# Kernel optimization log

Measured on AMD Instinct MI355X. Metric: run time of the kernel, lower is better.

## Reference

```python
import jax, jax.numpy as jnp
import numpy as np

N_NODES = 100000
N_EDGES = 3200000
D_FEAT = 128
HIDDEN = 128
BN_EPS = 1e-3  # Keras BatchNormalization default epsilon


def setup_inputs() -> dict:
    key = jax.random.key(0)
    k = jax.random.split(key, 8)
    H = jax.random.normal(k[0], (N_NODES, D_FEAT), dtype=jnp.float32)
    edge_src = jax.random.randint(k[1], (N_EDGES,), 0, N_NODES, dtype=jnp.int32)
    edge_dst = jax.random.randint(k[2], (N_EDGES,), 0, N_NODES, dtype=jnp.int32)
    edge_w = jax.random.uniform(k[3], (N_EDGES,), dtype=jnp.float32)
    # BatchNorm (inference-mode) parameters
    gamma = jnp.ones((D_FEAT,), dtype=jnp.float32)
    beta = jnp.zeros((D_FEAT,), dtype=jnp.float32)
    moving_mean = 0.1 * jax.random.normal(k[4], (D_FEAT,), dtype=jnp.float32)
    moving_var = jnp.abs(1.0 + 0.1 * jax.random.normal(k[5], (D_FEAT,), dtype=jnp.float32))
    # Dense layer params
    W = jax.random.normal(k[6], (D_FEAT, HIDDEN), dtype=jnp.float32) / np.sqrt(D_FEAT)
    b = jnp.zeros((HIDDEN,), dtype=jnp.float32)
    return {
        "H": H, "edge_src": edge_src, "edge_dst": edge_dst, "edge_w": edge_w,
        "gamma": gamma, "beta": beta, "moving_mean": moving_mean,
        "moving_var": moving_var, "W": W, "b": b, "num_nodes": N_NODES,
    }


def reference(H, edge_src, edge_dst, edge_w, gamma, beta, moving_mean, moving_var, W, b, num_nodes):
    # Sparse adjacency SpMM: h[dst] += w * H[src]
    msgs = H[edge_src] * edge_w[:, None]                      # [E, d]
    h = jax.ops.segment_sum(msgs, edge_dst, num_segments=num_nodes)  # [N, d]
    # BatchNorm (inference) -> Dropout (identity at inference) -> Dense + exact GELU
    h = (h - moving_mean) * jax.lax.rsqrt(moving_var + BN_EPS) * gamma + beta
    out = jax.nn.gelu(h @ W + b, approximate=False)           # [N, hidden]
    return out
```

## Files before the change

### kernel.cpp

```cpp
#include <hip/hip_runtime.h>
#include <math.h>


#define DF 128
#define SCAN_ELEMS 2048
#define BKSH 6
#define BKNODES (1 << BKSH)
#define NB 256
#define CAP 4096
#define CAP2 3072
#define PBLOCKS 512

typedef short short8 __attribute__((ext_vector_type(8)));
typedef float f32x4 __attribute__((ext_vector_type(4)));

__device__ __forceinline__ unsigned short f32_to_bf16_rne(float f) {
  unsigned u = __float_as_uint(f);
  return (unsigned short)((u + 0x7FFFu + ((u >> 16) & 1u)) >> 16);
}

__global__ __launch_bounds__(256) void scatter_kernel(
    const float* __restrict__ H, const int* __restrict__ esrc,
    const int* __restrict__ edst, const float* __restrict__ ew,
    float* __restrict__ h, int E) {
  int tid = blockIdx.x * blockDim.x + threadIdx.x;
  int e = tid >> 5;
  int lane = tid & 31;
  if (e >= E) return;
  int s = esrc[e];
  int d = edst[e];
  float w = ew[e];
  const float4* Hs = reinterpret_cast<const float4*>(H + (size_t)s * DF);
  float4 v = Hs[lane];
  float* hd = h + (size_t)d * DF + lane * 4;
  atomicAdd(hd + 0, v.x * w);
  atomicAdd(hd + 1, v.y * w);
  atomicAdd(hd + 2, v.z * w);
  atomicAdd(hd + 3, v.w * w);
}

__global__ __launch_bounds__(256) void prep_all_kernel(
    const float4* __restrict__ H4, ushort4* __restrict__ Hb, int n4,
    const float* __restrict__ W, const float* __restrict__ gamma,
    const float* __restrict__ beta, const float* __restrict__ mean,
    const float* __restrict__ var, const float* __restrict__ b,
    unsigned short* __restrict__ W2frag, float* __restrict__ bias2) {
  int idx = blockIdx.x * blockDim.x + threadIdx.x;
  if (idx < n4) {
    float4 v = H4[idx];
    ushort4 o;
    o.x = f32_to_bf16_rne(v.x);
    o.y = f32_to_bf16_rne(v.y);
    o.z = f32_to_bf16_rne(v.z);
    o.w = f32_to_bf16_rne(v.w);
    Hb[idx] = o;
  }
  if (idx < 16384) {
    int i = idx & 7;
    int l = (idx >> 3) & 63;
    int kt = (idx >> 9) & 3;
    int ct = idx >> 11;
    int k = kt * 32 + (l >> 4) * 8 + i;
    int c = ct * 16 + (l & 15);
    float s = gamma[k] * rsqrtf(var[k] + 1e-3f);
    W2frag[idx] = f32_to_bf16_rne(s * W[(size_t)k * DF + c]);
  } else if (idx < 16384 + DF) {
    int c = idx - 16384;
    float acc = b[c];
    for (int k = 0; k < DF; ++k) {
      float s = gamma[k] * rsqrtf(var[k] + 1e-3f);
      float t = beta[k] - mean[k] * s;
      acc += t * W[(size_t)k * DF + c];
    }
    bias2[c] = acc;
  }
}

__global__ __launch_bounds__(512) void hist_blk_kernel(
    const int* __restrict__ edst, int* __restrict__ gbase,
    int E, int nbk, int chunk) {
  extern __shared__ int hcnt[];
  int bblk = blockIdx.x;
  int t = threadIdx.x;
  for (int i = t; i < nbk; i += 512) hcnt[i] = 0;
  __syncthreads();
  int e0 = bblk * chunk;
  int e1 = min(E, e0 + chunk);
  for (int e = e0 + t; e < e1; e += 512)
    atomicAdd(&hcnt[edst[e] >> BKSH], 1);
  __syncthreads();
  for (int k = t; k < nbk; k += 512)
    gbase[(size_t)k * NB + bblk] = hcnt[k];
}

__global__ __launch_bounds__(256) void scan1_kernel(
    int* __restrict__ data, int* __restrict__ bsum, int n) {
  __shared__ int s[256];
  int t = threadIdx.x;
  int base = blockIdx.x * SCAN_ELEMS + t * 8;
  int v[8];
  int tsum = 0;
#pragma unroll
  for (int k = 0; k < 8; ++k) {
    v[k] = (base + k < n) ? data[base + k] : 0;
    tsum += v[k];
  }
  s[t] = tsum;
  __syncthreads();
  for (int off = 1; off < 256; off <<= 1) {
    int tmp = (t >= off) ? s[t - off] : 0;
    __syncthreads();
    s[t] += tmp;
    __syncthreads();
  }
  int run = s[t] - tsum;
#pragma unroll
  for (int k = 0; k < 8; ++k) {
    if (base + k < n) data[base + k] = run;
    run += v[k];
  }
  if (t == 255) bsum[blockIdx.x] = s[255];
}

__global__ __launch_bounds__(256) void scan23_kernel(
    int* __restrict__ data, const int* __restrict__ bsum, int n, int nbA) {
  __shared__ int s[256];
  int t = threadIdx.x;
  int v = (t < nbA) ? bsum[t] : 0;
  s[t] = v;
  __syncthreads();
  for (int off = 1; off < 256; off <<= 1) {
    int tmp = (t >= off) ? s[t - off] : 0;
    __syncthreads();
    s[t] += tmp;
    __syncthreads();
  }
  int i = blockIdx.x * 256 + t;
  if (i < n) {
    int blk = i >> 11;
    int add = (blk == 0) ? 0 : s[blk - 1];
    data[i] += add;
  }
  if (blockIdx.x == 0 && t == 0) data[n] = s[nbA - 1];
}

__global__ __launch_bounds__(512) void scatter_blk_kernel(
    const int* __restrict__ esrc, const int* __restrict__ edst,
    const float* __restrict__ ew, const int* __restrict__ gbase,
    uint2* __restrict__ payload, int E, int nbk, int chunk) {
  extern __shared__ int cur[];
  int bblk = blockIdx.x;
  int t = threadIdx.x;
  for (int k = t; k < nbk; k += 512) cur[k] = gbase[(size_t)k * NB + bblk];
  __syncthreads();
  int e0 = bblk * chunk;
  int e1 = min(E, e0 + chunk);
  for (int e = e0 + t; e < e1; e += 512) {
    int d = edst[e];
    int k = d >> BKSH;
    int pos = atomicAdd(&cur[k], 1);
    uint2 v;
    v.x = (unsigned)esrc[e] | ((unsigned)(d & (BKNODES - 1)) << 17);
    v.y = __float_as_uint(ew[e]);
    payload[pos] = v;
  }
}

__global__ __launch_bounds__(1024, 8) void reorder_pull_kernel(
    const unsigned* __restrict__ Hb, const uint2* __restrict__ payload,
    const int* __restrict__ gbase, unsigned* __restrict__ hb_out,
    int* __restrict__ ctr, int N, int nbk) {
  __shared__ uint2 sorted[CAP2];
  __shared__ int cnt[BKNODES];
  __shared__ int scn[BKNODES];
  __shared__ int cur[BKNODES];
  __shared__ int s_bk;
  int t = threadIdx.x;
  int wid = t >> 6;
  int lane = t & 63;
  int half = lane >> 5;
  int sub = lane & 31;
  const uint2* __restrict__ Hb2 = (const uint2*)Hb;

  for (;;) {
    if (t == 0) s_bk = atomicAdd(ctr, 1);
    __syncthreads();
    int bk = s_bk;
    if (bk >= nbk) return;
    int base = gbase[(size_t)bk * NB];
    int end  = gbase[(size_t)(bk + 1) * NB];
    int len = end - base;

    if (len <= CAP2) {
      if (t < BKNODES) cnt[t] = 0;
      __syncthreads();
      for (int j = t; j < len; j += 1024)
        atomicAdd(&cnt[payload[base + j].x >> 17], 1);
      __syncthreads();
      if (t < BKNODES) scn[t] = cnt[t];
      __syncthreads();
      for (int off = 1; off < BKNODES; off <<= 1) {
        int tmp = (t < BKNODES && t >= off) ? scn[t - off] : 0;
        __syncthreads();
        if (t < BKNODES) scn[t] += tmp;
        __syncthreads();
      }
      if (t < BKNODES) cur[t] = scn[t] - cnt[t];
      __syncthreads();
      for (int j = t; j < len; j += 1024) {
        uint2 m = payload[base + j];
        int pos = atomicAdd(&cur[m.x >> 17], 1);
        uint2 o;
        o.x = m.x & 0x1FFFFu;
        o.y = m.y;
        sorted[pos] = o;
      }
      __syncthreads();

#pragma unroll
      for (int i = 0; i < 4; ++i) {
        int dl = wid * 4 + i;
        int node = (bk << BKSH) + dl;
        if (node >= N) break;
        int s1 = scn[dl];
        int s0 = s1 - cnt[dl];
        float a0 = 0.0f, a1 = 0.0f, a2 = 0.0f, a3 = 0.0f;
        int j = s0;
        for (; j + 16 <= s1; j += 16) {
          uint2 mm[8], rr[8];
#pragma unroll
          for (int k = 0; k < 8; ++k) mm[k] = sorted[j + 2 * k + half];
#pragma unroll
          for (int k = 0; k < 8; ++k)
            rr[k] = Hb2[(size_t)mm[k].x * 32 + sub];
#pragma unroll
          for (int k = 0; k < 8; ++k) {
            float w = __uint_as_float(mm[k].y);
            a0 = fmaf(__uint_as_float(rr[k].x << 16), w, a0);
            a1 = fmaf(__uint_as_float(rr[k].x & 0xFFFF0000u), w, a1);
            a2 = fmaf(__uint_as_float(rr[k].y << 16), w, a2);
            a3 = fmaf(__uint_as_float(rr[k].y & 0xFFFF0000u), w, a3);
          }
        }
        for (; j + 2 <= s1; j += 2) {
          uint2 m = sorted[j + half];
          uint2 r = Hb2[(size_t)m.x * 32 + sub];
          float w = __uint_as_float(m.y);
          a0 = fmaf(__uint_as_float(r.x << 16), w, a0);
          a1 = fmaf(__uint_as_float(r.x & 0xFFFF0000u), w, a1);
          a2 = fmaf(__uint_as_float(r.y << 16), w, a2);
          a3 = fmaf(__uint_as_float(r.y & 0xFFFF0000u), w, a3);
        }
        if (j < s1 && half == 0) {
          uint2 m = sorted[j];
          uint2 r = Hb2[(size_t)m.x * 32 + sub];
          float w = __uint_as_float(m.y);
          a0 = fmaf(__uint_as_float(r.x << 16), w, a0);
          a1 = fmaf(__uint_as_float(r.x & 0xFFFF0000u), w, a1);
          a2 = fmaf(__uint_as_float(r.y << 16), w, a2);
          a3 = fmaf(__uint_as_float(r.y & 0xFFFF0000u), w, a3);
        }
        a0 += __shfl_xor(a0, 32);
        a1 += __shfl_xor(a1, 32);
        a2 += __shfl_xor(a2, 32);
        a3 += __shfl_xor(a3, 32);
        if (half == 0) {
          uint2 o;
          o.x = (unsigned)f32_to_bf16_rne(a0) |
                ((unsigned)f32_to_bf16_rne(a1) << 16);
          o.y = (unsigned)f32_to_bf16_rne(a2) |
                ((unsigned)f32_to_bf16_rne(a3) << 16);
          ((uint2*)hb_out)[(size_t)node * 32 + sub] = o;
        }
      }
    } else {
      for (int i = 0; i < 4; ++i) {
        int dl = wid * 4 + i;
        int node = (bk << BKSH) + dl;
        if (node >= N) break;
        float ax = 0.0f, ay = 0.0f;
        for (int j = base; j < end; ++j) {
          uint2 m = payload[j];
          if ((int)(m.x >> 17) == dl) {
            float w = __uint_as_float(m.y);
            unsigned p = Hb[(size_t)(m.x & 0x1FFFFu) * 64 + lane];
            ax = fmaf(__uint_as_float(p << 16), w, ax);
            ay = fmaf(__uint_as_float(p & 0xFFFF0000u), w, ay);
          }
        }
        unsigned pack = (unsigned)f32_to_bf16_rne(ax) |
                        ((unsigned)f32_to_bf16_rne(ay) << 16);
        hb_out[(size_t)node * 64 + lane] = pack;
      }
    }
    __syncthreads();
  }
}

__global__ __launch_bounds__(256) void mfma_gemm_gelu_kernel(
    const unsigned short* __restrict__ hb,
    const unsigned short* __restrict__ W2frag,
    const float* __restrict__ bias2,
    float* __restrict__ out, int N, int ngrp) {
  __shared__ unsigned short sW[8 * 4 * 64 * 8];

  int t = threadIdx.x;
  {
    const uint4* src = (const uint4*)W2frag;
    uint4* dst = (uint4*)sW;
    for (int i = t; i < 2048; i += 256) dst[i] = src[i];
  }
  __syncthreads();

  int wid = t >> 6;
  int l = t & 63;
  const short8* wf = (const short8*)sW;
  int orow = (l >> 4) * 4;
  int ocol = l & 15;

#pragma unroll
  for (int g = 0; g < 2; ++g) {
    int grp = blockIdx.x * 2 + g;
    if (grp >= ngrp) break;
    int row0 = grp * 64 + wid * 16;

    int arow = row0 + (l & 15);
    if (arow >= N) arow = N - 1;
    const short8* hrow = (const short8*)(hb + (size_t)arow * DF);
    int asub = l >> 4;
    short8 a[4];
#pragma unroll
    for (int kt = 0; kt < 4; ++kt) a[kt] = hrow[kt * 4 + asub];

#pragma unroll
    for (int ct = 0; ct < 8; ++ct) {
      f32x4 acc = {0.0f, 0.0f, 0.0f, 0.0f};
#pragma unroll
      for (int kt = 0; kt < 4; ++kt) {
        short8 bfr = wf[(ct * 4 + kt) * 64 + l];
        acc = __builtin_amdgcn_mfma_f32_16x16x32_bf16(a[kt], bfr, acc, 0, 0, 0);
      }
      int col = ct * 16 + ocol;
      float bb = bias2[col];
#pragma unroll
      for (int r = 0; r < 4; ++r) {
        int row = row0 + orow + r;
        if (row < N) {
          float x = acc[r] + bb;
          float gv = 0.5f * x * (1.0f + erff(x * 0.70710678118654752440f));
          out[(size_t)row * DF + col] = gv;
        }
      }
    }
  }
}

__global__ __launch_bounds__(256) void reorder2_kernel(
    const uint2* __restrict__ payload, const int* __restrict__ gbase,
    uint2* __restrict__ csr, int* __restrict__ rowptr,
    int N, int nbk, int E) {
  __shared__ uint2 stage[CAP];
  __shared__ int cnt[BKNODES];
  __shared__ int s64[BKNODES];
  __shared__ int cur[BKNODES];
  int bk = blockIdx.x;
  int t = threadIdx.x;
  int base = gbase[(size_t)bk * NB];
  int end  = gbase[(size_t)(bk + 1) * NB];
  int len = end - base;
  bool fit = (len <= CAP);

  if (t < BKNODES) cnt[t] = 0;
  __syncthreads();
  if (fit) {
    for (int j = t; j < len; j += 256) {
      uint2 m = payload[base + j];
      stage[j] = m;
      atomicAdd(&cnt[m.x >> 17], 1);
    }
  } else {
    for (int j = t; j < len; j += 256)
      atomicAdd(&cnt[payload[base + j].x >> 17], 1);
  }
  __syncthreads();
  if (t < BKNODES) s64[t] = cnt[t];
  __syncthreads();
  for (int off = 1; off < BKNODES; off <<= 1) {
    int tmp = 0;
    if (t < BKNODES && t >= off) tmp = s64[t - off];
    __syncthreads();
    if (t < BKNODES) s64[t] += tmp;
    __syncthreads();
  }
  if (t < BKNODES) {
    int ex = s64[t] - cnt[t];
    cur[t] = ex;
    int node = (bk << BKSH) + t;
    if (node < N) rowptr[node] = base + ex;
  }
  if (bk == nbk - 1 && t == 0) rowptr[N] = E;
  __syncthreads();
  if (fit) {
    for (int j = t; j < len; j += 256) {
      uint2 m = stage[j];
      int dl = (int)(m.x >> 17);
      int pos = atomicAdd(&cur[dl], 1);
      uint2 o;
      o.x = m.x & 0x1FFFFu;
      o.y = m.y;
      csr[(size_t)base + pos] = o;
    }
  } else {
    for (int j = t; j < len; j += 256) {
      uint2 m = payload[base + j];
      int dl = (int)(m.x >> 17);
      int pos = atomicAdd(&cur[dl], 1);
      uint2 o;
      o.x = m.x & 0x1FFFFu;
      o.y = m.y;
      csr[(size_t)base + pos] = o;
    }
  }
}

__global__ __launch_bounds__(256) void pull_csr_f32_kernel(
    const float2* __restrict__ H2, const int* __restrict__ rowptr,
    const uint2* __restrict__ csr_sw, float* __restrict__ h, int N) {
  int wave = threadIdx.x >> 6;
  int lane = threadIdx.x & 63;
  int node = blockIdx.x * 4 + wave;
  if (node >= N) return;
  int rs = rowptr[node];
  int re = rowptr[node + 1];
  float ax = 0.0f, ay = 0.0f;
  for (int j = rs; j < re; ++j) {
    uint2 m = csr_sw[j];
    float w = __uint_as_float(m.y);
    float2 u = H2[(size_t)m.x * 64 + lane];
    ax = fmaf(u.x, w, ax);
    ay = fmaf(u.y, w, ay);
  }
  float2 r;
  r.x = ax;
  r.y = ay;
  reinterpret_cast<float2*>(h)[(size_t)node * 64 + lane] = r;
}

__global__ __launch_bounds__(256) void fused_bn_gemm_gelu(
    float* __restrict__ hout, const float* __restrict__ gamma,
    const float* __restrict__ beta, const float* __restrict__ mean,
    const float* __restrict__ var, const float* __restrict__ W,
    const float* __restrict__ b, int N) {
  __shared__ float s_s[DF];
  __shared__ float s_t[DF];
  __shared__ float s_hb[16][DF];
  __shared__ float s_W[32][DF];

  int t = threadIdx.x;
  if (t < DF) {
    float sv = gamma[t] * rsqrtf(var[t] + 1e-3f);
    s_s[t] = sv;
    s_t[t] = beta[t] - mean[t] * sv;
  }
  __syncthreads();

  int n0 = blockIdx.x * 16;
  for (int i = t; i < 16 * DF; i += 256) {
    int r = i >> 7;
    int c = i & (DF - 1);
    int node = n0 + r;
    float hv = (node < N) ? hout[(size_t)node * DF + c] : 0.0f;
    s_hb[r][c] = hv * s_s[c] + s_t[c];
  }

  float acc[8];
#pragma unroll
  for (int i = 0; i < 8; i++) acc[i] = 0.0f;

  int col = t & (DF - 1);
  int half = t >> 7;

  for (int kc = 0; kc < DF; kc += 32) {
    __syncthreads();
    for (int i = t; i < 32 * DF; i += 256) {
      int r = i >> 7;
      int c = i & (DF - 1);
      s_W[r][c] = W[(size_t)(kc + r) * DF + c];
    }
    __syncthreads();
#pragma unroll
    for (int kk = 0; kk < 32; kk++) {
      float wv = s_W[kk][col];
#pragma unroll
      for (int i = 0; i < 8; i++) {
        acc[i] += s_hb[half + i * 2][kc + kk] * wv;
      }
    }
  }

  float bb = b[col];
#pragma unroll
  for (int i = 0; i < 8; i++) {
    int node = n0 + half + i * 2;
    if (node < N) {
      float x = acc[i] + bb;
      float g = 0.5f * x * (1.0f + erff(x * 0.70710678118654752440f));
      hout[(size_t)node * DF + col] = g;
    }
  }
}

extern "C" void kernel_launch(void* const* d_in, const int* in_sizes, int n_in,
                              void* d_out, int out_size, void* d_ws, size_t ws_size,
                              hipStream_t stream) {
  const float* H     = (const float*)d_in[0];
  const int*   esrc  = (const int*)d_in[1];
  const int*   edst  = (const int*)d_in[2];
  const float* ew    = (const float*)d_in[3];
  const float* gamma = (const float*)d_in[4];
  const float* beta  = (const float*)d_in[5];
  const float* mean  = (const float*)d_in[6];
  const float* var   = (const float*)d_in[7];
  const float* W     = (const float*)d_in[8];
  const float* b     = (const float*)d_in[9];

  int N = in_sizes[0] / DF;
  int E = in_sizes[1];
  float* h = (float*)d_out;

  int nbk = (N + BKNODES - 1) / BKNODES;
  int NBKG = nbk * NB;
  int nbA = (NBKG + SCAN_ELEMS - 1) / SCAN_ELEMS;
  int chunk = (E + NB - 1) / NB;

  size_t off = 0;
  auto alloc = [&](size_t bytes) {
    size_t o = off;
    off += (bytes + 255) & ~(size_t)255;
    return o;
  };
  size_t o_gbase  = alloc((size_t)(NBKG + 1) * 4);
  size_t o_bsum   = alloc((size_t)(nbA + 1) * 4);
  size_t o_rowptr = alloc((size_t)(N + 1) * 4);
  size_t o_w2     = alloc((size_t)16384 * 2);
  size_t o_bias2  = alloc((size_t)DF * 4);
  size_t o_ctr    = alloc(256);
  size_t o_pl     = alloc((size_t)E * 8);
  size_t o_csr    = alloc((size_t)E * 8);
  size_t need_bin = off;
  size_t o_hb     = alloc((size_t)N * DF * 2);
  size_t need_bf16 = off;

  char* ws = (char*)d_ws;

  if (ws_size >= need_bin) {
    int* gbase   = (int*)(ws + o_gbase);
    int* bsum    = (int*)(ws + o_bsum);
    int* rowptr  = (int*)(ws + o_rowptr);
    unsigned short* W2frag = (unsigned short*)(ws + o_w2);
    float* bias2 = (float*)(ws + o_bias2);
    int* ctr     = (int*)(ws + o_ctr);
    uint2* payload = (uint2*)(ws + o_pl);
    uint2* csr     = (uint2*)(ws + o_csr);
    bool tierA = (ws_size >= need_bf16 && (size_t)N * DF * 2 <= (size_t)E * 8);

    size_t lds_bytes = (size_t)nbk * 4;

    if (tierA) {
      ushort4* Hb = (ushort4*)(ws + o_hb);
      int n4 = N * DF / 4;
      prep_all_kernel<<<(n4 + 255) / 256, 256, 0, stream>>>(
          (const float4*)H, Hb, n4, W, gamma, beta, mean, var, b, W2frag, bias2);
      hist_blk_kernel<<<NB, 512, lds_bytes, stream>>>(edst, gbase, E, nbk, chunk);
      scan1_kernel<<<nbA, 256, 0, stream>>>(gbase, bsum, NBKG);
      scan23_kernel<<<(NBKG + 255) / 256, 256, 0, stream>>>(gbase, bsum, NBKG, nbA);
      scatter_blk_kernel<<<NB, 512, lds_bytes, stream>>>(esrc, edst, ew, gbase,
                                                         payload, E, nbk, chunk);
      hipMemsetAsync(ctr, 0, 4, stream);
      unsigned* hb_out = (unsigned*)(ws + o_csr);
      int pgrid = min(PBLOCKS, nbk);
      reorder_pull_kernel<<<pgrid, 1024, 0, stream>>>(
          (const unsigned*)Hb, payload, gbase, hb_out, ctr, N, nbk);
      int ngrp = (N + 63) / 64;
      mfma_gemm_gelu_kernel<<<(ngrp + 1) / 2, 256, 0, stream>>>(
          (const unsigned short*)hb_out, W2frag, bias2, (float*)d_out, N, ngrp);
    } else {
      hist_blk_kernel<<<NB, 512, lds_bytes, stream>>>(edst, gbase, E, nbk, chunk);
      scan1_kernel<<<nbA, 256, 0, stream>>>(gbase, bsum, NBKG);
      scan23_kernel<<<(NBKG + 255) / 256, 256, 0, stream>>>(gbase, bsum, NBKG, nbA);
      scatter_blk_kernel<<<NB, 512, lds_bytes, stream>>>(esrc, edst, ew, gbase,
                                                         payload, E, nbk, chunk);
      reorder2_kernel<<<nbk, 256, 0, stream>>>(payload, gbase, csr, rowptr,
                                               N, nbk, E);
      pull_csr_f32_kernel<<<(N + 3) / 4, 256, 0, stream>>>(
          (const float2*)H, rowptr, csr, h, N);
      fused_bn_gemm_gelu<<<(N + 15) / 16, 256, 0, stream>>>(h, gamma, beta,
                                                            mean, var, W, b, N);
    }
  } else {
    hipMemsetAsync(d_out, 0, (size_t)out_size * sizeof(float), stream);
    long long threads = (long long)E * 32;
    long long grid = (threads + 255) / 256;
    scatter_kernel<<<(int)grid, 256, 0, stream>>>(H, esrc, edst, ew, h, E);
    fused_bn_gemm_gelu<<<(N + 15) / 16, 256, 0, stream>>>(h, gamma, beta,
                                                          mean, var, W, b, N);
  }
}
```

Baseline: 247.8 us.

## Stage bucket payload in LDS and gather full rows per wave with 4-byte loads

The bucket payload is now copied into a shared-memory staging buffer on the first pass, so the counting-sort scatter reads LDS instead of re-reading global memory. The per-node gather changes from half-wave 8-byte loads that cover two edges per instruction, followed by a cross-half shuffle reduction, to whole-wave 4-byte loads of one full 256-byte row per edge. This removes the shuffle and halves register accumulators, but doubles the number of gather load instructions and doubles LDS usage per block, which may reduce occupancy.

```diff
diff --git a/kernel.cpp b/kernel.cpp
--- a/kernel.cpp
+++ b/kernel.cpp
@@ -170,6 +170,7 @@
     const unsigned* __restrict__ Hb, const uint2* __restrict__ payload,
     const int* __restrict__ gbase, unsigned* __restrict__ hb_out,
     int* __restrict__ ctr, int N, int nbk) {
+  __shared__ uint2 stage[CAP2];
   __shared__ uint2 sorted[CAP2];
   __shared__ int cnt[BKNODES];
   __shared__ int scn[BKNODES];
@@ -178,9 +179,6 @@
   int t = threadIdx.x;
   int wid = t >> 6;
   int lane = t & 63;
-  int half = lane >> 5;
-  int sub = lane & 31;
-  const uint2* __restrict__ Hb2 = (const uint2*)Hb;
 
   for (;;) {
     if (t == 0) s_bk = atomicAdd(ctr, 1);
@@ -194,8 +192,11 @@
     if (len <= CAP2) {
       if (t < BKNODES) cnt[t] = 0;
       __syncthreads();
-      for (int j = t; j < len; j += 1024)
-        atomicAdd(&cnt[payload[base + j].x >> 17], 1);
+      for (int j = t; j < len; j += 1024) {
+        uint2 m = payload[base + j];
+        stage[j] = m;
+        atomicAdd(&cnt[m.x >> 17], 1);
+      }
       __syncthreads();
       if (t < BKNODES) scn[t] = cnt[t];
       __syncthreads();
@@ -208,7 +209,7 @@
       if (t < BKNODES) cur[t] = scn[t] - cnt[t];
       __syncthreads();
       for (int j = t; j < len; j += 1024) {
-        uint2 m = payload[base + j];
+        uint2 m = stage[j];
         int pos = atomicAdd(&cur[m.x >> 17], 1);
         uint2 o;
         o.x = m.x & 0x1FFFFu;
@@ -224,54 +225,36 @@
         if (node >= N) break;
         int s1 = scn[dl];
         int s0 = s1 - cnt[dl];
-        float a0 = 0.0f, a1 = 0.0f, a2 = 0.0f, a3 = 0.0f;
+        float ax = 0.0f, ay = 0.0f;
         int j = s0;
-        for (; j + 16 <= s1; j += 16) {
-          uint2 mm[8], rr[8];
-#pragma unroll
-          for (int k = 0; k < 8; ++k) mm[k] = sorted[j + 2 * k + half];
-#pragma unroll
-          for (int k = 0; k < 8; ++k)
-            rr[k] = Hb2[(size_t)mm[k].x * 32 + sub];
+        for (; j + 8 <= s1; j += 8) {
+          uint2 m[8];
+#pragma unroll
+          for (int k = 0; k < 8; ++k) m[k] = sorted[j + k];
+          float lo[8], hi[8];
 #pragma unroll
           for (int k = 0; k < 8; ++k) {
-            float w = __uint_as_float(mm[k].y);
-            a0 = fmaf(__uint_as_float(rr[k].x << 16), w, a0);
-            a1 = fmaf(__uint_as_float(rr[k].x & 0xFFFF0000u), w, a1);
-            a2 = fmaf(__uint_as_float(rr[k].y << 16), w, a2);
-            a3 = fmaf(__uint_as_float(rr[k].y & 0xFFFF0000u), w, a3);
+            unsigned p = Hb[(size_t)m[k].x * 64 + lane];
+            lo[k] = __uint_as_float(p << 16);
+            hi[k] = __uint_as_float(p & 0xFFFF0000u);
+          }
+#pragma unroll
+          for (int k = 0; k < 8; ++k) {
+            float w = __uint_as_float(m[k].y);
+            ax = fmaf(lo[k], w, ax);
+            ay = fmaf(hi[k], w, ay);
           }
         }
-        for (; j + 2 <= s1; j += 2) {
-          uint2 m = sorted[j + half];
-          uint2 r = Hb2[(size_t)m.x * 32 + sub];
+        for (; j < s1; ++j) {
+          uint2 m = sorted[j];
           float w = __uint_as_float(m.y);
-          a0 = fmaf(__uint_as_float(r.x << 16), w, a0);
-          a1 = fmaf(__uint_as_float(r.x & 0xFFFF0000u), w, a1);
-          a2 = fmaf(__uint_as_float(r.y << 16), w, a2);
-          a3 = fmaf(__uint_as_float(r.y & 0xFFFF0000u), w, a3);
+          unsigned p = Hb[(size_t)m.x * 64 + lane];
+          ax = fmaf(__uint_as_float(p << 16), w, ax);
+          ay = fmaf(__uint_as_float(p & 0xFFFF0000u), w, ay);
         }
-        if (j < s1 && half == 0) {
-          uint2 m = sorted[j];
-          uint2 r = Hb2[(size_t)m.x * 32 + sub];
-          float w = __uint_as_float(m.y);
-          a0 = fmaf(__uint_as_float(r.x << 16), w, a0);
-          a1 = fmaf(__uint_as_float(r.x & 0xFFFF0000u), w, a1);
-          a2 = fmaf(__uint_as_float(r.y << 16), w, a2);
-          a3 = fmaf(__uint_as_float(r.y & 0xFFFF0000u), w, a3);
-        }
-        a0 += __shfl_xor(a0, 32);
-        a1 += __shfl_xor(a1, 32);
-        a2 += __shfl_xor(a2, 32);
-        a3 += __shfl_xor(a3, 32);
-        if (half == 0) {
-          uint2 o;
-          o.x = (unsigned)f32_to_bf16_rne(a0) |
-                ((unsigned)f32_to_bf16_rne(a1) << 16);
-          o.y = (unsigned)f32_to_bf16_rne(a2) |
-                ((unsigned)f32_to_bf16_rne(a3) << 16);
-          ((uint2*)hb_out)[(size_t)node * 32 + sub] = o;
-        }
+        unsigned pack = (unsigned)f32_to_bf16_rne(ax) |
+                        ((unsigned)f32_to_bf16_rne(ay) << 16);
+        hb_out[(size_t)node * 64 + lane] = pack;
       }
     } else {
       for (int i = 0; i < 4; ++i) {
```

Result: faster. 233.1 us (-6.0%).
